# Kernel tuning notes

Hardware: AMD Instinct MI355X
Metric: run time of the kernel (lower is better)

Reference implementation:

```python
import jax, jax.numpy as jnp
import numpy as np

BS, Q, NC, T = 32, 600, 152, 32


def cxcywh_to_xyxy(b):
    cx, cy, w, h = b[..., 0], b[..., 1], b[..., 2], b[..., 3]
    return jnp.stack([cx - 0.5 * w, cy - 0.5 * h, cx + 0.5 * w, cy + 0.5 * h], axis=-1)


def generalized_box_iou(b1, b2):
    # b1: [N,4], b2: [M,4] in xyxy. Returns [N,M] GIoU.
    area1 = (b1[:, 2] - b1[:, 0]) * (b1[:, 3] - b1[:, 1])
    area2 = (b2[:, 2] - b2[:, 0]) * (b2[:, 3] - b2[:, 1])
    lt = jnp.maximum(b1[:, None, :2], b2[None, :, :2])
    rb = jnp.minimum(b1[:, None, 2:], b2[None, :, 2:])
    wh = jnp.clip(rb - lt, 0.0)
    inter = wh[..., 0] * wh[..., 1]
    union = area1[:, None] + area2[None, :] - inter
    iou = inter / union
    ltc = jnp.minimum(b1[:, None, :2], b2[None, :, :2])
    rbc = jnp.maximum(b1[:, None, 2:], b2[None, :, 2:])
    whc = jnp.clip(rbc - ltc, 0.0)
    areac = whc[..., 0] * whc[..., 1]
    return iou - (areac - union) / areac


def build_cost(logits, boxes, tgt_ids, tgt_bbox, wc=1.0, wb=1.0, wg=1.0):
    # logits [bs,Q,NC], boxes [bs,Q,4] cxcywh; tgt_ids [bs*T], tgt_bbox [bs*T,4].
    bs, q, _ = logits.shape
    prob = jax.nn.softmax(logits.reshape(bs * q, -1), axis=-1)
    cost_class = -prob[:, tgt_ids]                                  # [bs*Q, bs*T]
    ob = boxes.reshape(bs * q, 4)
    cost_bbox = jnp.abs(ob[:, None, :] - tgt_bbox[None, :, :]).sum(-1)  # L1 cdist
    cost_giou = -generalized_box_iou(cxcywh_to_xyxy(ob), cxcywh_to_xyxy(tgt_bbox))
    C = wb * cost_bbox + wc * cost_class + wg * cost_giou
    return C.reshape(bs, q, -1)


def lsa(cost):
    # Exact rectangular linear sum assignment (Jonker-Volgenant shortest
    # augmenting path with potentials). cost: np [n, m], n <= m.
    # Returns (rows, cols): matched pairs sorted by col index.
    n, m = cost.shape
    INF = 1e18
    u = np.zeros(n + 1)
    v = np.zeros(m + 1)
    p = np.zeros(m + 1, dtype=np.int64)   # p[j] = row matched to col j (1-based)
    way = np.zeros(m + 1, dtype=np.int64)
    for i in range(1, n + 1):
        p[0] = i
        j0 = 0
        minv = np.full(m + 1, INF)
        used = np.zeros(m + 1, dtype=bool)
        while True:
            used[j0] = True
            i0 = p[j0]
            free = np.where(~used)[0]
            cur = cost[i0 - 1, free - 1] - u[i0] - v[free]
            better = cur < minv[free]
            minv[free] = np.where(better, cur, minv[free])
            way[free] = np.where(better, j0, way[free])
            k = int(np.argmin(minv[free]))
            delta = minv[free][k]
            j1 = int(free[k])
            uidx = np.where(used)[0]
            u[p[uidx]] += delta
            v[uidx] -= delta
            minv[free] -= delta
            j0 = j1
            if p[j0] == 0:
                break
        while j0 != 0:
            j1 = int(way[j0])
            p[j0] = p[j1]
            j0 = j1
    cols = np.where(p[1:] != 0)[0]
    rows = p[1:][cols] - 1
    return rows, cols


def match(C_np):
    # C_np: [bs, Q, bs*T]; use diagonal target blocks like torch split-by-sizes.
    pred_idx, tgt_idx = [], []
    for b in range(BS):
        block = C_np[b, :, b * T:(b + 1) * T].T      # [T, Q], T <= Q
        r, c = lsa(block)                            # r: target idx, c: pred idx
        pred_idx.append(c)
        tgt_idx.append(r)
    return jnp.asarray(np.stack(pred_idx)), jnp.asarray(np.stack(tgt_idx))


def setup_inputs() -> dict:
    key = jax.random.key(0)
    ks = jax.random.split(key, 8)
    return {
        "pred_sub_logits": jax.random.normal(ks[0], (BS, Q, NC), jnp.float32),
        "pred_obj_logits": jax.random.normal(ks[1], (BS, Q, NC), jnp.float32),
        "pred_boxes_sub": jax.random.uniform(ks[2], (BS, Q, 4), jnp.float32),
        "pred_boxes_obj": jax.random.uniform(ks[3], (BS, Q, 4), jnp.float32),
        "tgt_sub_bbox": jax.random.uniform(ks[4], (BS, T, 4), jnp.float32),
        "tgt_obj_bbox": jax.random.uniform(ks[5], (BS, T, 4), jnp.float32),
        "tgt_sub_ids": jax.random.randint(ks[6], (BS, T), 0, NC, jnp.int64),
        "tgt_obj_ids": jax.random.randint(ks[7], (BS, T), 0, NC, jnp.int64),
    }


def reference(pred_sub_logits, pred_obj_logits, pred_boxes_sub, pred_boxes_obj,
              tgt_sub_bbox, tgt_obj_bbox, tgt_sub_ids, tgt_obj_ids):
    ids_s = tgt_sub_ids.reshape(-1)
    ids_o = tgt_obj_ids.reshape(-1)
    C_sub = build_cost(pred_sub_logits, pred_boxes_sub, ids_s, tgt_sub_bbox.reshape(-1, 4))
    C_obj = build_cost(pred_obj_logits, pred_boxes_obj, ids_o, tgt_obj_bbox.reshape(-1, 4))
    # Host-side exact Hungarian per batch element (mirrors scipy
    # linear_sum_assignment on the CPU-transferred cost matrix).
    Cs_np = np.asarray(C_sub, dtype=np.float64)
    Co_np = np.asarray(C_obj, dtype=np.float64)
    ps, ts = match(Cs_np)
    po, to = match(Co_np)
    return (C_sub, C_obj, ps, ts, po, to)
```

## Files before the change

### kernel.cpp

```cpp
#include <hip/hip_runtime.h>
#include <math.h>

#define BS 32
#define Q  600
#define NC 152
#define T  32
#define MT (BS*T)
#define CM_SIZE ((size_t)BS*Q*MT)
#define NSLOT 10
#define FBIG 1e30f

typedef float vfloat4 __attribute__((ext_vector_type(4)));

__global__ __launch_bounds__(256) void cost_kernel(
    const float* __restrict__ logits_s, const float* __restrict__ logits_o,
    const float* __restrict__ boxes_s,  const float* __restrict__ boxes_o,
    const float* __restrict__ tbb_s,    const float* __restrict__ tbb_o,
    const int*   __restrict__ tids_s,   const int*   __restrict__ tids_o,
    float* __restrict__ C_s, float* __restrict__ C_o,
    float* __restrict__ blockT, int use_staged)
{
    const int w = threadIdx.x >> 6, lane = threadIdx.x & 63;
    const int rowg = blockIdx.x * 4 + w;
    const int mat = rowg / (BS * Q);
    const int r   = rowg % (BS * Q);
    const int b = r / Q, q = r % Q;

    const float* logits = mat ? logits_o : logits_s;
    const float* boxes  = mat ? boxes_o  : boxes_s;
    const float* tbb    = mat ? tbb_o    : tbb_s;
    const int*   tids   = mat ? tids_o   : tids_s;
    float* C = mat ? C_o : C_s;

    const float* lrow = logits + (size_t)r * NC;
    const float l0 = (lane       < NC) ? lrow[lane]       : -INFINITY;
    const float l1 = (lane + 64  < NC) ? lrow[lane + 64]  : -INFINITY;
    const float l2 = (lane + 128 < NC) ? lrow[lane + 128] : -INFINITY;
    float m = fmaxf(l0, fmaxf(l1, l2));
    #pragma unroll
    for (int off = 32; off > 0; off >>= 1) m = fmaxf(m, __shfl_xor(m, off));
    const float e0 = expf(l0 - m), e1 = expf(l1 - m), e2 = expf(l2 - m);
    float s = e0 + e1 + e2;
    #pragma unroll
    for (int off = 32; off > 0; off >>= 1) s += __shfl_xor(s, off);
    const float inv = 1.0f / s;

    __shared__ float sprob[4][NC];
    if (lane       < NC) sprob[w][lane]       = e0 * inv;
    if (lane + 64  < NC) sprob[w][lane + 64]  = e1 * inv;
    if (lane + 128 < NC) sprob[w][lane + 128] = e2 * inv;
    __syncthreads();

    const float4 ob = ((const float4*)boxes)[r];
    const float ocx = ob.x, ocy = ob.y, ow = ob.z, oh = ob.w;
    const float ox1 = ocx - 0.5f*ow, oy1 = ocy - 0.5f*oh;
    const float ox2 = ocx + 0.5f*ow, oy2 = ocy + 0.5f*oh;
    const float area1 = ow * oh;

    float* Crow = C + (size_t)r * MT;
    float* bT   = blockT + ((size_t)mat*BS + b) * T * Q;

    #pragma unroll
    for (int it = 0; it < 4; ++it) {
        const int t0 = it*256 + lane*4;
        const int4 cls4 = ((const int4*)tids)[t0 >> 2];
        const bool stg = use_staged && ((t0 >> 5) == b);
        vfloat4 res;
        #pragma unroll
        for (int k = 0; k < 4; ++k) {
            const int t = t0 + k;
            const int cls = (&cls4.x)[k];
            const float cc = -sprob[w][cls];

            const float4 tb = ((const float4*)tbb)[t];
            const float cb = fabsf(ocx-tb.x) + fabsf(ocy-tb.y)
                           + fabsf(ow -tb.z) + fabsf(oh -tb.w);

            const float tx1 = fmaf(-0.5f, tb.z, tb.x), ty1 = fmaf(-0.5f, tb.w, tb.y);
            const float tx2 = fmaf( 0.5f, tb.z, tb.x), ty2 = fmaf( 0.5f, tb.w, tb.y);
            const float area2 = tb.z * tb.w;

            const float ltx = fmaxf(ox1,tx1), lty = fmaxf(oy1,ty1);
            const float rbx = fminf(ox2,tx2), rby = fminf(oy2,ty2);
            const float iw = fmaxf(rbx-ltx, 0.0f), ih = fmaxf(rby-lty, 0.0f);
            const float inter = iw*ih;
            const float uni = area1 + area2 - inter;

            const float cx1 = fminf(ox1,tx1), cy1 = fminf(oy1,ty1);
            const float cx2 = fmaxf(ox2,tx2), cy2 = fmaxf(oy2,ty2);
            const float areac = (cx2-cx1)*(cy2-cy1);

            const float giou = inter * __builtin_amdgcn_rcpf(uni)
                             - (areac - uni) * __builtin_amdgcn_rcpf(areac);

            const float cost = cb + cc - giou;
            res[k] = cost;
            if (stg) bT[(size_t)(t & 31)*Q + q] = cost;
        }
        __builtin_nontemporal_store(res, (vfloat4*)(Crow + t0));
    }
}

__device__ __forceinline__ unsigned long long wave_min_u64(unsigned long long k) {
  #define STAGE(CTRL, RMASK) { \
    int lo = (int)(unsigned)(k & 0xffffffffull); \
    int hi = (int)(unsigned)(k >> 32); \
    int plo = __builtin_amdgcn_update_dpp(lo, lo, CTRL, RMASK, 0xF, false); \
    int phi = __builtin_amdgcn_update_dpp(hi, hi, CTRL, RMASK, 0xF, false); \
    unsigned long long p = ((unsigned long long)(unsigned)phi << 32) | (unsigned)plo; \
    k = (p < k) ? p : k; }
  STAGE(0xB1, 0xF)
  STAGE(0x4E, 0xF)
  STAGE(0x141, 0xF)
  STAGE(0x140, 0xF)
  STAGE(0x142, 0xA)
  STAGE(0x143, 0xC)
  #undef STAGE
  unsigned lo63 = (unsigned)__builtin_amdgcn_readlane((int)(unsigned)(k & 0xffffffffull), 63);
  unsigned hi63 = (unsigned)__builtin_amdgcn_readlane((int)(unsigned)(k >> 32), 63);
  return ((unsigned long long)hi63 << 32) | lo63;
}

__device__ __forceinline__ unsigned f32_sortable(float f) {
  unsigned u = __float_as_uint(f);
  return u ^ ((unsigned)((int)u >> 31) | 0x80000000u);
}
__device__ __forceinline__ float f32_unsortable(unsigned s) {
  unsigned m = (unsigned)((int)(~s) >> 31) | 0x80000000u;
  return __uint_as_float(s ^ m);
}

__global__ __launch_bounds__(64) void lsa_kernel(
    const float* __restrict__ blockT, const float* __restrict__ Cbase,
    float* __restrict__ idx_out, int use_staged)
{
    const int prob = blockIdx.x;
    const int mat = prob >> 5, b = prob & 31;
    const int lane = threadIdx.x;

    __shared__ float clds[T * Q];
    __shared__ float u_s[T + 1];
    __shared__ int   p_s[Q + 1];

    if (use_staged) {
        const float4* src = (const float4*)(blockT + (size_t)prob * T * Q);
        float4* dst = (float4*)clds;
        for (int idx = lane; idx < (T*Q)/4; idx += 64)
            dst[idx] = src[idx];
    } else {
        const float* cbk = Cbase + (size_t)mat*CM_SIZE + (size_t)b*Q*MT + (size_t)b*T;
        for (int t = 0; t < T; ++t)
            for (int q = lane; q < Q; q += 64)
                clds[t*Q + q] = cbk[(size_t)q * MT + t];
    }

    for (int j = lane; j <= Q; j += 64) p_s[j] = 0;
    if (lane <= T) u_s[lane] = 0.0f;
    __syncthreads();

    float vreg[NSLOT], minv[NSLOT];
    int   wayreg[NSLOT], low[NSLOT];
    #pragma unroll
    for (int c = 0; c < NSLOT; ++c) vreg[c] = 0.0f;

    for (int i = 1; i <= T; ++i) {
        #pragma unroll
        for (int c = 0; c < NSLOT; ++c) {
            const int q0 = c*64 + lane;
            minv[c] = FBIG;
            wayreg[c] = 0;
            low[c] = (q0 < Q) ? (((q0 + 1) << 6) | p_s[q0 + 1]) : 0x3FFFFF;
        }
        unsigned usedmask = 0;
        float Dcum = 0.0f;
        int j0 = 0, i0 = i, jfin;

        while (true) {
            const float u0 = u_s[i0];
            const float* crow = clds + (i0 - 1) * Q;

            float cst[NSLOT];
            #pragma unroll
            for (int c = 0; c < NSLOT; ++c) {
                const int q0 = c*64 + lane;
                cst[c] = (q0 < Q) ? crow[q0] : FBIG;
            }
            const float sh = Dcum - u0;

            unsigned long long k[NSLOT];
            #pragma unroll
            for (int c = 0; c < NSLOT; ++c) {
                const bool fre = !((usedmask >> c) & 1u);
                const float cur = (cst[c] - vreg[c]) + sh;
                const bool upd = fre && (cur < minv[c]);
                wayreg[c] = upd ? j0 : wayreg[c];
                minv[c]   = upd ? cur : minv[c];
                const float mv = fre ? minv[c] : FBIG;
                k[c] = ((unsigned long long)f32_sortable(mv) << 22) | (unsigned)low[c];
            }
            #pragma unroll
            for (int c = 0; c < 5; ++c) k[c] = (k[c+5] < k[c]) ? k[c+5] : k[c];
            k[0] = (k[3] < k[0]) ? k[3] : k[0];
            k[1] = (k[4] < k[1]) ? k[4] : k[1];
            k[0] = (k[2] < k[0]) ? k[2] : k[0];
            k[0] = (k[1] < k[0]) ? k[1] : k[0];

            unsigned long long key = wave_min_u64(k[0]);

            Dcum = f32_unsortable((unsigned)(key >> 22));
            const int j1  = (int)((key >> 6) & 0x3FF);
            const int pj1 = (int)(key & 0x3F);

            if (pj1 == 0) { jfin = j1; break; }
            const int owner1 = (j1 - 1) & 63, slot1 = (j1 - 1) >> 6;
            if (lane == owner1) usedmask |= 1u << slot1;
            j0 = j1; i0 = pj1;
        }

        const float Dfin = Dcum;
        #pragma unroll
        for (int c = 0; c < NSLOT; ++c) {
            if ((usedmask >> c) & 1u) {
                const float dec = Dfin - minv[c];
                vreg[c] -= dec;
                u_s[low[c] & 63] += dec;
            }
        }
        if (lane == 0) u_s[i] += Dfin;
        __syncthreads();

        int jj = jfin;
        while (jj) {
            const int owner = (jj - 1) & 63, slot = (jj - 1) >> 6;
            int wv = 0;
            #pragma unroll
            for (int c = 0; c < NSLOT; ++c) if (slot == c) wv = wayreg[c];
            const int jw = __shfl(wv, owner);
            int newp;
            if (jw == 0) newp = i;
            else {
                const int ow2 = (jw - 1) & 63, sl2 = (jw - 1) >> 6;
                int pv2 = 0;
                #pragma unroll
                for (int c = 0; c < NSLOT; ++c) if (sl2 == c) pv2 = low[c] & 63;
                newp = __shfl(pv2, ow2);
            }
            if (lane == 0) p_s[jj] = newp;
            jj = jw;
        }
        __syncthreads();
    }

    float* pred = idx_out + (size_t)mat * 2 * BS * T;
    float* tgt  = pred + BS * T;
    int base = 0;
    #pragma unroll
    for (int c = 0; c < NSLOT; ++c) {
        const int q0 = c*64 + lane;
        const int pj = (q0 < Q) ? p_s[q0 + 1] : 0;
        const bool mtch = (q0 < Q) && (pj != 0);
        const unsigned long long mask = __ballot(mtch);
        if (mtch) {
            const int pos = base + __popcll(mask & ((1ull << lane) - 1ull));
            pred[b*T + pos] = (float)q0;
            tgt [b*T + pos] = (float)(pj - 1);
        }
        base += __popcll(mask);
    }
}

extern "C" void kernel_launch(void* const* d_in, const int* in_sizes, int n_in,
                              void* d_out, int out_size, void* d_ws, size_t ws_size,
                              hipStream_t stream) {
    const float* logits_s = (const float*)d_in[0];
    const float* logits_o = (const float*)d_in[1];
    const float* boxes_s  = (const float*)d_in[2];
    const float* boxes_o  = (const float*)d_in[3];
    const float* tbb_s    = (const float*)d_in[4];
    const float* tbb_o    = (const float*)d_in[5];
    const int*   tids_s   = (const int*)d_in[6];
    const int*   tids_o   = (const int*)d_in[7];

    float* out = (float*)d_out;
    float* C_s = out;
    float* C_o = out + CM_SIZE;
    float* idx_out = out + 2*CM_SIZE;

    const size_t staged_bytes = (size_t)2*BS*T*Q*sizeof(float);
    const int use_staged = (ws_size >= staged_bytes) ? 1 : 0;
    float* blockT = (float*)d_ws;

    cost_kernel<<<(2*BS*Q)/4, 256, 0, stream>>>(logits_s, logits_o, boxes_s, boxes_o,
                                                tbb_s, tbb_o, tids_s, tids_o,
                                                C_s, C_o, blockT, use_staged);

    lsa_kernel<<<64, 64, 0, stream>>>(blockT, C_s, idx_out, use_staged);
}
```

Baseline: 304.7 us.

## Fuse cost and LSA kernels so Hungarian blocks overlap full cost-matrix writes

Merges the cost kernel and the assignment kernel into one launch. The first 64 blocks each recompute their own diagonal 32x600 cost block into scratch and then run the shortest-augmenting-path solver from global memory at raised wave priority. The remaining blocks write the full cost matrices in parallel. This removes the serial dependency between writing the full matrix and starting the solver, and drops the shared-memory staging copy. The cost is duplicated softmax and pair-cost work for the diagonal blocks, and solver reads now come from global or L2 memory instead of LDS.

```diff
diff --git a/kernel.cpp b/kernel.cpp
--- a/kernel.cpp
+++ b/kernel.cpp
@@ -9,8 +9,288 @@
 #define CM_SIZE ((size_t)BS*Q*MT)
 #define NSLOT 10
 #define FBIG 1e30f
+#define NPROB 64
+#define LSA_BLOCKS 64
 
 typedef float vfloat4 __attribute__((ext_vector_type(4)));
+
+__device__ __forceinline__ float pair_cost(const float4 ob, const float4 tb, const float cc) {
+    const float ocx = ob.x, ocy = ob.y, ow = ob.z, oh = ob.w;
+    const float ox1 = ocx - 0.5f*ow, oy1 = ocy - 0.5f*oh;
+    const float ox2 = ocx + 0.5f*ow, oy2 = ocy + 0.5f*oh;
+    const float area1 = ow * oh;
+
+    const float cb = fabsf(ocx-tb.x) + fabsf(ocy-tb.y)
+                   + fabsf(ow -tb.z) + fabsf(oh -tb.w);
+
+    const float tx1 = fmaf(-0.5f, tb.z, tb.x), ty1 = fmaf(-0.5f, tb.w, tb.y);
+    const float tx2 = fmaf( 0.5f, tb.z, tb.x), ty2 = fmaf( 0.5f, tb.w, tb.y);
+    const float area2 = tb.z * tb.w;
+
+    const float ltx = fmaxf(ox1,tx1), lty = fmaxf(oy1,ty1);
+    const float rbx = fminf(ox2,tx2), rby = fminf(oy2,ty2);
+    const float iw = fmaxf(rbx-ltx, 0.0f), ih = fmaxf(rby-lty, 0.0f);
+    const float inter = iw*ih;
+    const float uni = area1 + area2 - inter;
+
+    const float cx1 = fminf(ox1,tx1), cy1 = fminf(oy1,ty1);
+    const float cx2 = fmaxf(ox2,tx2), cy2 = fmaxf(oy2,ty2);
+    const float areac = (cx2-cx1)*(cy2-cy1);
+
+    const float giou = inter * __builtin_amdgcn_rcpf(uni)
+                     - (areac - uni) * __builtin_amdgcn_rcpf(areac);
+    return cb + cc - giou;
+}
+
+__device__ __forceinline__ void softmax_row(const float* __restrict__ lrow,
+                                            const int lane, float* sp) {
+    const float l0 = (lane       < NC) ? lrow[lane]       : -INFINITY;
+    const float l1 = (lane + 64  < NC) ? lrow[lane + 64]  : -INFINITY;
+    const float l2 = (lane + 128 < NC) ? lrow[lane + 128] : -INFINITY;
+    float m = fmaxf(l0, fmaxf(l1, l2));
+    #pragma unroll
+    for (int off = 32; off > 0; off >>= 1) m = fmaxf(m, __shfl_xor(m, off));
+    const float e0 = expf(l0 - m), e1 = expf(l1 - m), e2 = expf(l2 - m);
+    float s = e0 + e1 + e2;
+    #pragma unroll
+    for (int off = 32; off > 0; off >>= 1) s += __shfl_xor(s, off);
+    const float inv = 1.0f / s;
+    if (lane       < NC) sp[lane]       = e0 * inv;
+    if (lane + 64  < NC) sp[lane + 64]  = e1 * inv;
+    if (lane + 128 < NC) sp[lane + 128] = e2 * inv;
+}
+
+__device__ __forceinline__ unsigned f32_sortable(float f) {
+  unsigned u = __float_as_uint(f);
+  return u ^ ((unsigned)((int)u >> 31) | 0x80000000u);
+}
+__device__ __forceinline__ float f32_unsortable(unsigned s) {
+  unsigned m = (unsigned)((int)(~s) >> 31) | 0x80000000u;
+  return __uint_as_float(s ^ m);
+}
+
+__device__ __forceinline__ unsigned wave_min_u32(unsigned x) {
+  int v = (int)x;
+  #define ST(CTRL, RMASK) { \
+    int p = __builtin_amdgcn_update_dpp(v, v, CTRL, RMASK, 0xF, false); \
+    v = ((unsigned)p < (unsigned)v) ? p : v; }
+  ST(0xB1, 0xF)
+  ST(0x4E, 0xF)
+  ST(0x141, 0xF)
+  ST(0x140, 0xF)
+  ST(0x142, 0xA)
+  ST(0x143, 0xC)
+  #undef ST
+  return (unsigned)__builtin_amdgcn_readlane(v, 63);
+}
+
+__device__ __forceinline__ unsigned long long wave_min_u64(unsigned long long k) {
+  #define STAGE(CTRL, RMASK) { \
+    int lo = (int)(unsigned)(k & 0xffffffffull); \
+    int hi = (int)(unsigned)(k >> 32); \
+    int plo = __builtin_amdgcn_update_dpp(lo, lo, CTRL, RMASK, 0xF, false); \
+    int phi = __builtin_amdgcn_update_dpp(hi, hi, CTRL, RMASK, 0xF, false); \
+    unsigned long long p = ((unsigned long long)(unsigned)phi << 32) | (unsigned)plo; \
+    k = (p < k) ? p : k; }
+  STAGE(0xB1, 0xF) STAGE(0x4E, 0xF) STAGE(0x141, 0xF)
+  STAGE(0x140, 0xF) STAGE(0x142, 0xA) STAGE(0x143, 0xC)
+  #undef STAGE
+  unsigned lo63 = (unsigned)__builtin_amdgcn_readlane((int)(unsigned)(k & 0xffffffffull), 63);
+  unsigned hi63 = (unsigned)__builtin_amdgcn_readlane((int)(unsigned)(k >> 32), 63);
+  return ((unsigned long long)hi63 << 32) | lo63;
+}
+
+__global__ __launch_bounds__(256, 4) void fused_kernel(
+    const float* __restrict__ logits_s, const float* __restrict__ logits_o,
+    const float* __restrict__ boxes_s,  const float* __restrict__ boxes_o,
+    const float* __restrict__ tbb_s,    const float* __restrict__ tbb_o,
+    const int*   __restrict__ tids_s,   const int*   __restrict__ tids_o,
+    float* __restrict__ C_s, float* __restrict__ C_o,
+    float* __restrict__ scratch, float* __restrict__ idx_out)
+{
+    const int tid = threadIdx.x, w = tid >> 6, lane = tid & 63;
+
+    __shared__ float  sprob[4][NC];
+    __shared__ float  u_s[T + 1];
+    __shared__ int    p_s[Q + 1];
+    __shared__ float4 tb_sh[T];
+    __shared__ int    cls_sh[T];
+
+    if (blockIdx.x >= LSA_BLOCKS) {
+        const int rowg = (blockIdx.x - LSA_BLOCKS) * 4 + w;
+        const int mat = rowg / (BS * Q);
+        const int r   = rowg % (BS * Q);
+
+        const float* logits = mat ? logits_o : logits_s;
+        const float* boxes  = mat ? boxes_o  : boxes_s;
+        const float* tbb    = mat ? tbb_o    : tbb_s;
+        const int*   tids   = mat ? tids_o   : tids_s;
+        float* C = mat ? C_o : C_s;
+
+        softmax_row(logits + (size_t)r * NC, lane, sprob[w]);
+
+        const float4 ob = ((const float4*)boxes)[r];
+        float* Crow = C + (size_t)r * MT;
+
+        #pragma unroll
+        for (int it = 0; it < 4; ++it) {
+            const int t0 = it*256 + lane*4;
+            const int4 cls4 = ((const int4*)tids)[t0 >> 2];
+            vfloat4 res;
+            #pragma unroll
+            for (int k = 0; k < 4; ++k) {
+                const int t = t0 + k;
+                const float cc = -sprob[w][(&cls4.x)[k]];
+                const float4 tb = ((const float4*)tbb)[t];
+                res[k] = pair_cost(ob, tb, cc);
+            }
+            __builtin_nontemporal_store(res, (vfloat4*)(Crow + t0));
+        }
+        return;
+    }
+
+    const int prob = blockIdx.x;
+    const int mat = prob >> 5, b = prob & 31;
+    const float* logits = mat ? logits_o : logits_s;
+    const float* boxes  = mat ? boxes_o  : boxes_s;
+    const float* tbb    = mat ? tbb_o    : tbb_s;
+    const int*   tids   = mat ? tids_o   : tids_s;
+    float* blk = scratch + (size_t)prob * T * Q;
+
+    if (tid < T) {
+        tb_sh[tid]  = ((const float4*)tbb)[b*T + tid];
+        cls_sh[tid] = tids[b*T + tid];
+    }
+    for (int j = tid; j <= Q; j += 256) p_s[j] = 0;
+    if (tid <= T) u_s[tid] = 0.0f;
+    __syncthreads();
+
+    for (int q = w; q < Q; q += 4) {
+        const int r = b*Q + q;
+        softmax_row(logits + (size_t)r * NC, lane, sprob[w]);
+        const float4 ob = ((const float4*)boxes)[r];
+        if (lane < T) {
+            const float cc = -sprob[w][cls_sh[lane]];
+            blk[(size_t)lane * Q + q] = pair_cost(ob, tb_sh[lane], cc);
+        }
+    }
+    __syncthreads();
+    if (w != 0) return;
+
+    __builtin_amdgcn_s_setprio(3);
+
+    float vreg[NSLOT], minv[NSLOT];
+    int   wayreg[NSLOT], low[NSLOT];
+    #pragma unroll
+    for (int c = 0; c < NSLOT; ++c) vreg[c] = 0.0f;
+
+    for (int i = 1; i <= T; ++i) {
+        #pragma unroll
+        for (int c = 0; c < NSLOT; ++c) {
+            const int q0 = c*64 + lane;
+            minv[c] = FBIG;
+            wayreg[c] = 0;
+            low[c] = (q0 < Q) ? (((q0 + 1) << 6) | p_s[q0 + 1]) : 0x3FFFFF;
+        }
+        unsigned usedmask = 0;
+        float Dcum = 0.0f;
+        int j0 = 0, i0 = i, jfin;
+
+        while (true) {
+            const float u0 = u_s[i0];
+            const float* crow = blk + (size_t)(i0 - 1) * Q;
+
+            float cst[NSLOT];
+            #pragma unroll
+            for (int c = 0; c < NSLOT; ++c) {
+                const int q0 = c*64 + lane;
+                cst[c] = (q0 < Q) ? crow[q0] : FBIG;
+            }
+            const float sh = Dcum - u0;
+
+            float bm[NSLOT];
+            #pragma unroll
+            for (int c = 0; c < NSLOT; ++c) {
+                const bool fre = !((usedmask >> c) & 1u);
+                const float cur = (cst[c] - vreg[c]) + sh;
+                const bool upd = fre && (cur < minv[c]);
+                wayreg[c] = upd ? j0 : wayreg[c];
+                minv[c]   = upd ? cur : minv[c];
+                bm[c] = fre ? minv[c] : FBIG;
+            }
+            const float m0 = fminf(bm[0], fminf(bm[1], bm[2]));
+            const float m1 = fminf(bm[3], fminf(bm[4], bm[5]));
+            const float m2 = fminf(bm[6], fminf(bm[7], bm[8]));
+            const float best = fminf(fminf(m0, m1), fminf(m2, bm[9]));
+            int blow = 0x3FFFFF;
+            #pragma unroll
+            for (int c = NSLOT - 1; c >= 0; --c) blow = (bm[c] == best) ? low[c] : blow;
+
+            const unsigned sb = f32_sortable(best);
+            const unsigned gb = wave_min_u32(sb);
+            const unsigned long long mask = __ballot(sb == gb);
+            const int src = __ffsll(mask) - 1;
+            const int blow_w = __builtin_amdgcn_readlane(blow, src);
+
+            Dcum = f32_unsortable(gb);
+            const int j1  = (blow_w >> 6) & 0x3FF;
+            const int pj1 = blow_w & 0x3F;
+
+            if (pj1 == 0) { jfin = j1; break; }
+            const int owner1 = (j1 - 1) & 63, slot1 = (j1 - 1) >> 6;
+            if (lane == owner1) usedmask |= 1u << slot1;
+            j0 = j1; i0 = pj1;
+        }
+
+        const float Dfin = Dcum;
+        #pragma unroll
+        for (int c = 0; c < NSLOT; ++c) {
+            if ((usedmask >> c) & 1u) {
+                const float dec = Dfin - minv[c];
+                vreg[c] -= dec;
+                u_s[low[c] & 63] += dec;
+            }
+        }
+        if (lane == 0) u_s[i] += Dfin;
+
+        int jj = jfin;
+        while (jj) {
+            const int owner = (jj - 1) & 63, slot = (jj - 1) >> 6;
+            int wv = 0;
+            #pragma unroll
+            for (int c = 0; c < NSLOT; ++c) if (slot == c) wv = wayreg[c];
+            const int jw = __shfl(wv, owner);
+            int newp;
+            if (jw == 0) newp = i;
+            else {
+                const int ow2 = (jw - 1) & 63, sl2 = (jw - 1) >> 6;
+                int pv2 = 0;
+                #pragma unroll
+                for (int c = 0; c < NSLOT; ++c) if (sl2 == c) pv2 = low[c] & 63;
+                newp = __shfl(pv2, ow2);
+            }
+            if (lane == 0) p_s[jj] = newp;
+            jj = jw;
+        }
+    }
+
+    float* pred = idx_out + (size_t)mat * 2 * BS * T;
+    float* tgt  = pred + BS * T;
+    int base = 0;
+    #pragma unroll
+    for (int c = 0; c < NSLOT; ++c) {
+        const int q0 = c*64 + lane;
+        const int pj = (q0 < Q) ? p_s[q0 + 1] : 0;
+        const bool mtch = (q0 < Q) && (pj != 0);
+        const unsigned long long mask = __ballot(mtch);
+        if (mtch) {
+            const int pos = base + __popcll(mask & ((1ull << lane) - 1ull));
+            pred[b*T + pos] = (float)q0;
+            tgt [b*T + pos] = (float)(pj - 1);
+        }
+        base += __popcll(mask);
+    }
+}
 
 __global__ __launch_bounds__(256) void cost_kernel(
     const float* __restrict__ logits_s, const float* __restrict__ logits_o,
@@ -32,31 +312,11 @@
     const int*   tids   = mat ? tids_o   : tids_s;
     float* C = mat ? C_o : C_s;
 
-    const float* lrow = logits + (size_t)r * NC;
-    const float l0 = (lane       < NC) ? lrow[lane]       : -INFINITY;
-    const float l1 = (lane + 64  < NC) ? lrow[lane + 64]  : -INFINITY;
-    const float l2 = (lane + 128 < NC) ? lrow[lane + 128] : -INFINITY;
-    float m = fmaxf(l0, fmaxf(l1, l2));
-    #pragma unroll
-    for (int off = 32; off > 0; off >>= 1) m = fmaxf(m, __shfl_xor(m, off));
-    const float e0 = expf(l0 - m), e1 = expf(l1 - m), e2 = expf(l2 - m);
-    float s = e0 + e1 + e2;
-    #pragma unroll
-    for (int off = 32; off > 0; off >>= 1) s += __shfl_xor(s, off);
-    const float inv = 1.0f / s;
-
     __shared__ float sprob[4][NC];
-    if (lane       < NC) sprob[w][lane]       = e0 * inv;
-    if (lane + 64  < NC) sprob[w][lane + 64]  = e1 * inv;
-    if (lane + 128 < NC) sprob[w][lane + 128] = e2 * inv;
+    softmax_row(logits + (size_t)r * NC, lane, sprob[w]);
     __syncthreads();
 
     const float4 ob = ((const float4*)boxes)[r];
-    const float ocx = ob.x, ocy = ob.y, ow = ob.z, oh = ob.w;
-    const float ox1 = ocx - 0.5f*ow, oy1 = ocy - 0.5f*oh;
-    const float ox2 = ocx + 0.5f*ow, oy2 = ocy + 0.5f*oh;
-    const float area1 = ow * oh;
-
     float* Crow = C + (size_t)r * MT;
     float* bT   = blockT + ((size_t)mat*BS + b) * T * Q;
 
@@ -69,65 +329,14 @@
         #pragma unroll
         for (int k = 0; k < 4; ++k) {
             const int t = t0 + k;
-            const int cls = (&cls4.x)[k];
-            const float cc = -sprob[w][cls];
-
+            const float cc = -sprob[w][(&cls4.x)[k]];
             const float4 tb = ((const float4*)tbb)[t];
-            const float cb = fabsf(ocx-tb.x) + fabsf(ocy-tb.y)
-                           + fabsf(ow -tb.z) + fabsf(oh -tb.w);
-
-            const float tx1 = fmaf(-0.5f, tb.z, tb.x), ty1 = fmaf(-0.5f, tb.w, tb.y);
-            const float tx2 = fmaf( 0.5f, tb.z, tb.x), ty2 = fmaf( 0.5f, tb.w, tb.y);
-            const float area2 = tb.z * tb.w;
-
-            const float ltx = fmaxf(ox1,tx1), lty = fmaxf(oy1,ty1);
-            const float rbx = fminf(ox2,tx2), rby = fminf(oy2,ty2);
-            const float iw = fmaxf(rbx-ltx, 0.0f), ih = fmaxf(rby-lty, 0.0f);
-            const float inter = iw*ih;
-            const float uni = area1 + area2 - inter;
-
-            const float cx1 = fminf(ox1,tx1), cy1 = fminf(oy1,ty1);
-            const float cx2 = fmaxf(ox2,tx2), cy2 = fmaxf(oy2,ty2);
-            const float areac = (cx2-cx1)*(cy2-cy1);
-
-            const float giou = inter * __builtin_amdgcn_rcpf(uni)
-                             - (areac - uni) * __builtin_amdgcn_rcpf(areac);
-
-            const float cost = cb + cc - giou;
+            const float cost = pair_cost(ob, tb, cc);
             res[k] = cost;
             if (stg) bT[(size_t)(t & 31)*Q + q] = cost;
         }
         __builtin_nontemporal_store(res, (vfloat4*)(Crow + t0));
     }
-}
-
-__device__ __forceinline__ unsigned long long wave_min_u64(unsigned long long k) {
-  #define STAGE(CTRL, RMASK) { \
-    int lo = (int)(unsigned)(k & 0xffffffffull); \
-    int hi = (int)(unsigned)(k >> 32); \
-    int plo = __builtin_amdgcn_update_dpp(lo, lo, CTRL, RMASK, 0xF, false); \
-    int phi = __builtin_amdgcn_update_dpp(hi, hi, CTRL, RMASK, 0xF, false); \
-    unsigned long long p = ((unsigned long long)(unsigned)phi << 32) | (unsigned)plo; \
-    k = (p < k) ? p : k; }
-  STAGE(0xB1, 0xF)
-  STAGE(0x4E, 0xF)
-  STAGE(0x141, 0xF)
-  STAGE(0x140, 0xF)
-  STAGE(0x142, 0xA)
-  STAGE(0x143, 0xC)
-  #undef STAGE
-  unsigned lo63 = (unsigned)__builtin_amdgcn_readlane((int)(unsigned)(k & 0xffffffffull), 63);
-  unsigned hi63 = (unsigned)__builtin_amdgcn_readlane((int)(unsigned)(k >> 32), 63);
-  return ((unsigned long long)hi63 << 32) | lo63;
-}
-
-__device__ __forceinline__ unsigned f32_sortable(float f) {
-  unsigned u = __float_as_uint(f);
-  return u ^ ((unsigned)((int)u >> 31) | 0x80000000u);
-}
-__device__ __forceinline__ float f32_unsortable(unsigned s) {
-  unsigned m = (unsigned)((int)(~s) >> 31) | 0x80000000u;
-  return __uint_as_float(s ^ m);
 }
 
 __global__ __launch_bounds__(64) void lsa_kernel(
@@ -145,8 +354,7 @@
     if (use_staged) {
         const float4* src = (const float4*)(blockT + (size_t)prob * T * Q);
         float4* dst = (float4*)clds;
-        for (int idx = lane; idx < (T*Q)/4; idx += 64)
-            dst[idx] = src[idx];
+        for (int idx = lane; idx < (T*Q)/4; idx += 64) dst[idx] = src[idx];
     } else {
         const float* cbk = Cbase + (size_t)mat*CM_SIZE + (size_t)b*Q*MT + (size_t)b*T;
         for (int t = 0; t < T; ++t)
@@ -286,13 +494,15 @@
     float* C_o = out + CM_SIZE;
     float* idx_out = out + 2*CM_SIZE;
 
-    const size_t staged_bytes = (size_t)2*BS*T*Q*sizeof(float);
-    const int use_staged = (ws_size >= staged_bytes) ? 1 : 0;
-    float* blockT = (float*)d_ws;
-
-    cost_kernel<<<(2*BS*Q)/4, 256, 0, stream>>>(logits_s, logits_o, boxes_s, boxes_o,
-                                                tbb_s, tbb_o, tids_s, tids_o,
-                                                C_s, C_o, blockT, use_staged);
-
-    lsa_kernel<<<64, 64, 0, stream>>>(blockT, C_s, idx_out, use_staged);
-}
+    const size_t need = (size_t)NPROB * T * Q * sizeof(float);
+    if (ws_size >= need) {
+        fused_kernel<<<LSA_BLOCKS + (2*BS*Q)/4, 256, 0, stream>>>(
+            logits_s, logits_o, boxes_s, boxes_o, tbb_s, tbb_o, tids_s, tids_o,
+            C_s, C_o, (float*)d_ws, idx_out);
+    } else {
+        cost_kernel<<<(2*BS*Q)/4, 256, 0, stream>>>(logits_s, logits_o, boxes_s, boxes_o,
+                                                    tbb_s, tbb_o, tids_s, tids_o,
+                                                    C_s, C_o, nullptr, 0);
+        lsa_kernel<<<64, 64, 0, stream>>>(nullptr, C_s, idx_out, 0);
+    }
+}
```

New measurement: 405.9 us. 33.2% more time.

## Use 32-bit wave min reduction and keep column matches in registers

Applied to the files above, without the earlier changes.

The argmin in the Hungarian inner loop now does a per-lane float min, then a 32-bit DPP wave reduction on the sortable value. A ballot resolves which lane holds the winner, and a second reduction on the packed index runs only when there is a tie. This replaces the 64-bit packed-key reduction and cuts the DPP ops per step. The column-to-row match array moves from LDS into per-lane registers (pcol), which removes two __syncthreads per row. The softmax also switches to fast __expf, which risks small precision differences in the cost values.

```diff
diff --git a/kernel.cpp b/kernel.cpp
--- a/kernel.cpp
+++ b/kernel.cpp
@@ -39,7 +39,7 @@
     float m = fmaxf(l0, fmaxf(l1, l2));
     #pragma unroll
     for (int off = 32; off > 0; off >>= 1) m = fmaxf(m, __shfl_xor(m, off));
-    const float e0 = expf(l0 - m), e1 = expf(l1 - m), e2 = expf(l2 - m);
+    const float e0 = __expf(l0 - m), e1 = __expf(l1 - m), e2 = __expf(l2 - m);
     float s = e0 + e1 + e2;
     #pragma unroll
     for (int off = 32; off > 0; off >>= 1) s += __shfl_xor(s, off);
@@ -101,24 +101,19 @@
     }
 }
 
-__device__ __forceinline__ unsigned long long wave_min_u64(unsigned long long k) {
-  #define STAGE(CTRL, RMASK) { \
-    int lo = (int)(unsigned)(k & 0xffffffffull); \
-    int hi = (int)(unsigned)(k >> 32); \
-    int plo = __builtin_amdgcn_update_dpp(lo, lo, CTRL, RMASK, 0xF, false); \
-    int phi = __builtin_amdgcn_update_dpp(hi, hi, CTRL, RMASK, 0xF, false); \
-    unsigned long long p = ((unsigned long long)(unsigned)phi << 32) | (unsigned)plo; \
-    k = (p < k) ? p : k; }
-  STAGE(0xB1, 0xF)
-  STAGE(0x4E, 0xF)
-  STAGE(0x141, 0xF)
-  STAGE(0x140, 0xF)
-  STAGE(0x142, 0xA)
-  STAGE(0x143, 0xC)
-  #undef STAGE
-  unsigned lo63 = (unsigned)__builtin_amdgcn_readlane((int)(unsigned)(k & 0xffffffffull), 63);
-  unsigned hi63 = (unsigned)__builtin_amdgcn_readlane((int)(unsigned)(k >> 32), 63);
-  return ((unsigned long long)hi63 << 32) | lo63;
+__device__ __forceinline__ unsigned wave_min_u32(unsigned x) {
+  int v = (int)x;
+  #define ST(CTRL, RMASK) { \
+    int p = __builtin_amdgcn_update_dpp(v, v, CTRL, RMASK, 0xF, false); \
+    v = ((unsigned)p < (unsigned)v) ? p : v; }
+  ST(0xB1, 0xF)
+  ST(0x4E, 0xF)
+  ST(0x141, 0xF)
+  ST(0x140, 0xF)
+  ST(0x142, 0xA)
+  ST(0x143, 0xC)
+  #undef ST
+  return (unsigned)__builtin_amdgcn_readlane(v, 63);
 }
 
 __device__ __forceinline__ unsigned f32_sortable(float f) {
@@ -140,7 +135,6 @@
 
     __shared__ float clds[T * Q];
     __shared__ float u_s[T + 1];
-    __shared__ int   p_s[Q + 1];
 
     if (use_staged) {
         const float4* src = (const float4*)(blockT + (size_t)prob * T * Q);
@@ -153,15 +147,14 @@
             for (int q = lane; q < Q; q += 64)
                 clds[t*Q + q] = cbk[(size_t)q * MT + t];
     }
-
-    for (int j = lane; j <= Q; j += 64) p_s[j] = 0;
     if (lane <= T) u_s[lane] = 0.0f;
     __syncthreads();
 
     float vreg[NSLOT], minv[NSLOT];
     int   wayreg[NSLOT], low[NSLOT];
-    #pragma unroll
-    for (int c = 0; c < NSLOT; ++c) vreg[c] = 0.0f;
+    int   pcol[NSLOT];
+    #pragma unroll
+    for (int c = 0; c < NSLOT; ++c) { vreg[c] = 0.0f; pcol[c] = 0; }
 
     for (int i = 1; i <= T; ++i) {
         #pragma unroll
@@ -169,7 +162,7 @@
             const int q0 = c*64 + lane;
             minv[c] = FBIG;
             wayreg[c] = 0;
-            low[c] = (q0 < Q) ? (((q0 + 1) << 6) | p_s[q0 + 1]) : 0x3FFFFF;
+            low[c] = (q0 < Q) ? (((q0 + 1) << 6) | pcol[c]) : 0x3FFFFF;
         }
         unsigned usedmask = 0;
         float Dcum = 0.0f;
@@ -187,7 +180,7 @@
             }
             const float sh = Dcum - u0;
 
-            unsigned long long k[NSLOT];
+            float bm[NSLOT];
             #pragma unroll
             for (int c = 0; c < NSLOT; ++c) {
                 const bool fre = !((usedmask >> c) & 1u);
@@ -195,21 +188,30 @@
                 const bool upd = fre && (cur < minv[c]);
                 wayreg[c] = upd ? j0 : wayreg[c];
                 minv[c]   = upd ? cur : minv[c];
-                const float mv = fre ? minv[c] : FBIG;
-                k[c] = ((unsigned long long)f32_sortable(mv) << 22) | (unsigned)low[c];
-            }
+                bm[c] = fre ? minv[c] : FBIG;
+            }
+            const float m0 = fminf(bm[0], fminf(bm[1], bm[2]));
+            const float m1 = fminf(bm[3], fminf(bm[4], bm[5]));
+            const float m2 = fminf(bm[6], fminf(bm[7], bm[8]));
+            const float best = fminf(fminf(m0, m1), fminf(m2, bm[9]));
+            int blow = 0x3FFFFF;
             #pragma unroll
-            for (int c = 0; c < 5; ++c) k[c] = (k[c+5] < k[c]) ? k[c+5] : k[c];
-            k[0] = (k[3] < k[0]) ? k[3] : k[0];
-            k[1] = (k[4] < k[1]) ? k[4] : k[1];
-            k[0] = (k[2] < k[0]) ? k[2] : k[0];
-            k[0] = (k[1] < k[0]) ? k[1] : k[0];
-
-            unsigned long long key = wave_min_u64(k[0]);
-
-            Dcum = f32_unsortable((unsigned)(key >> 22));
-            const int j1  = (int)((key >> 6) & 0x3FF);
-            const int pj1 = (int)(key & 0x3F);
+            for (int c = NSLOT - 1; c >= 0; --c) blow = (bm[c] == best) ? low[c] : blow;
+
+            const unsigned sb = f32_sortable(best);
+            const unsigned gb = wave_min_u32(sb);
+            const unsigned long long mask = __ballot(sb == gb);
+            int blow_w;
+            if (__popcll(mask) == 1) {
+                blow_w = __builtin_amdgcn_readlane(blow, __ffsll(mask) - 1);
+            } else {
+                const unsigned cand = (sb == gb) ? (unsigned)blow : 0x3FFFFFu;
+                blow_w = (int)wave_min_u32(cand);
+            }
+
+            Dcum = f32_unsortable(gb);
+            const int j1  = (blow_w >> 6) & 0x3FF;
+            const int pj1 = blow_w & 0x3F;
 
             if (pj1 == 0) { jfin = j1; break; }
             const int owner1 = (j1 - 1) & 63, slot1 = (j1 - 1) >> 6;
@@ -227,7 +229,6 @@
             }
         }
         if (lane == 0) u_s[i] += Dfin;
-        __syncthreads();
 
         int jj = jfin;
         while (jj) {
@@ -245,10 +246,12 @@
                 for (int c = 0; c < NSLOT; ++c) if (sl2 == c) pv2 = low[c] & 63;
                 newp = __shfl(pv2, ow2);
             }
-            if (lane == 0) p_s[jj] = newp;
+            if (lane == owner) {
+                #pragma unroll
+                for (int c = 0; c < NSLOT; ++c) if (slot == c) pcol[c] = newp;
+            }
             jj = jw;
         }
-        __syncthreads();
     }
 
     float* pred = idx_out + (size_t)mat * 2 * BS * T;
@@ -257,7 +260,7 @@
     #pragma unroll
     for (int c = 0; c < NSLOT; ++c) {
         const int q0 = c*64 + lane;
-        const int pj = (q0 < Q) ? p_s[q0 + 1] : 0;
+        const int pj = (q0 < Q) ? pcol[c] : 0;
         const bool mtch = (q0 < Q) && (pj != 0);
         const unsigned long long mask = __ballot(mtch);
         if (mtch) {
```

After: 290.7 us. -4.6%, faster.
